# Optimization experiments

Hardware: AMD Instinct MI355X
Metric: run time of the kernel (lower is better)

## Reference

```python
import jax, jax.numpy as jnp
import numpy as np

N_KNOTS = 10
NEXPERTS = 1
NC = 8
STEP = 1.0 / (N_KNOTS - 1.0)
BN_EPS = 1e-5


def _spline_matrix(n, step):
    # natural cubic spline second-derivative solve matrix (precalc in torch code)
    mat = 4.0 * np.eye(n - 2)
    np.fill_diagonal(mat[1:, :-1], 1.0)
    np.fill_diagonal(mat[:-1, 1:], 1.0)
    A = 6.0 * np.linalg.inv(mat) / step ** 2
    z = np.zeros((1, n - 2))
    A = np.vstack([z, A, z])                      # [n, n-2]
    B = np.zeros((n - 2, n))
    np.fill_diagonal(B, 1.0)
    np.fill_diagonal(B[:, 1:], -2.0)
    np.fill_diagonal(B[:, 2:], 1.0)
    return jnp.asarray(A @ B, dtype=jnp.float32)  # [n, n]


def _conv(x, w, b, stride=2):
    y = jax.lax.conv_general_dilated(x, w, (stride, stride), 'VALID',
                                     dimension_numbers=('NCHW', 'OIHW', 'NCHW'))
    return y + b[None, :, None, None]


def _bn(x, g, be):
    # training-mode batchnorm (module default)
    m = x.mean(axis=(0, 2, 3), keepdims=True)
    v = x.var(axis=(0, 2, 3), keepdims=True)
    return g[None, :, None, None] * (x - m) * jax.lax.rsqrt(v + BN_EPS) + be[None, :, None, None]


def _interpolate(ys, mat):
    # ys: [..., n] -> cubic coeffs a,b,c,d each [..., n-1]
    h = STEP
    M = jnp.einsum('ij,...j->...i', mat, ys)
    a = (M[..., 1:] - M[..., :-1]) / (6.0 * h)
    b = M[..., :-1] / 2.0
    c = (ys[..., 1:] - ys[..., :-1]) / h - (M[..., 1:] + 2.0 * M[..., :-1]) * (h / 6.0)
    d = ys[..., :-1]
    return a, b, c, d


def _apply(coeffs, x):
    # coeffs: 4-tuple each [..., n-1]; x: [..., P] with matching leading dims
    a, b, c, d = coeffs
    xi = jnp.clip(jnp.floor(x / STEP), 0.0, N_KNOTS - 2.0)
    xf = x - xi * STEP
    idx = xi.astype(jnp.int32)
    ag = jnp.take_along_axis(a, idx, axis=-1)
    bg = jnp.take_along_axis(b, idx, axis=-1)
    cg = jnp.take_along_axis(c, idx, axis=-1)
    dg = jnp.take_along_axis(d, idx, axis=-1)
    return ((ag * xf + bg) * xf + cg) * xf + dg


def forward(x, w1, b1, w2, b2, g2, be2, w3, b3, g3, be3, w4, b4, g4, be4,
            w5, b5, g5, be5, fc1_w, fc1_b, fc2_w, fc2_b):
    B, C, H, W = x.shape
    small = x if (H, W) == (256, 256) else jax.image.resize(x, (B, C, 256, 256), 'bilinear')
    h = jax.nn.relu(_conv(small, w1, b1))
    h = _bn(jax.nn.relu(_conv(h, w2, b2)), g2, be2)
    h = _bn(jax.nn.relu(_conv(h, w3, b3)), g3, be3)
    h = _bn(jax.nn.relu(_conv(h, w4, b4)), g4, be4)
    h = _bn(jax.nn.relu(_conv(h, w5, b5)), g5, be5)   # [B, 16nc, 7, 7]
    h = h.mean(axis=(2, 3))                            # avgpool 7 -> [B, 16nc]
    h = jax.nn.relu(h @ fc1_w.T + fc1_b)
    ys = (h @ fc2_w.T + fc2_b).reshape(B, NEXPERTS, 3, N_KNOTS)
    identity = jnp.arange(N_KNOTS, dtype=jnp.float32) / (N_KNOTS - 1.0)
    ysn = ys + identity                                # residual spline
    mat = _spline_matrix(N_KNOTS, STEP)
    coeffs = _interpolate(ysn, mat)                    # each [B,E,3,n-1]
    # per-pixel spline eval at original resolution
    px = jnp.broadcast_to(x.reshape(B, 1, 3, H * W), (B, NEXPERTS, 3, H * W))
    out = _apply(coeffs, px).reshape(B, NEXPERTS, 3, H, W)
    out = jnp.transpose(out, (1, 0, 2, 3, 4))          # [E,B,3,H,W]
    # spline curves sampled at xs = arange(0,1,1/255) (255 points; detached in torch)
    xs = jnp.arange(0.0, 1.0, 1.0 / 255.0, dtype=jnp.float32)
    xs_b = jnp.broadcast_to(xs, (B, NEXPERTS, 3, xs.shape[0]))
    splines = jnp.transpose(_apply(coeffs, xs_b), (1, 0, 2, 3))  # [E,B,3,255]
    return out, splines


def setup_inputs() -> dict:
    key = jax.random.key(0)
    ks = jax.random.split(key, 16)
    n, nc, E = N_KNOTS, NC, NEXPERTS
    d = {}
    d['x'] = jax.random.uniform(ks[0], (8, 3, 1024, 1024), dtype=jnp.float32)
    d['w1'] = jax.random.normal(ks[1], (nc, 3, 3, 3), jnp.float32) * 0.1
    d['b1'] = jnp.zeros((nc,), jnp.float32)
    chans = [nc, 2 * nc, 4 * nc, 8 * nc, 16 * nc]
    for i, (ci, co) in enumerate(zip(chans[:-1], chans[1:]), start=2):
        d[f'w{i}'] = jax.random.normal(ks[i], (co, ci, 3, 3), jnp.float32) * 0.1
        d[f'b{i}'] = jnp.zeros((co,), jnp.float32)
        d[f'g{i}'] = jnp.ones((co,), jnp.float32)
        d[f'be{i}'] = jnp.zeros((co,), jnp.float32)
    d['fc1_w'] = jax.random.normal(ks[10], (16 * nc, 16 * nc), jnp.float32) * 0.05
    d['fc1_b'] = jnp.zeros((16 * nc,), jnp.float32)
    d['fc2_w'] = jax.random.normal(ks[11], (3 * n * E, 16 * nc), jnp.float32) * 0.05
    d['fc2_b'] = jnp.zeros((3 * n * E,), jnp.float32)
    return d


def reference(x, w1, b1, w2, b2, g2, be2, w3, b3, g3, be3, w4, b4, g4, be4,
              w5, b5, g5, be5, fc1_w, fc1_b, fc2_w, fc2_b):
    return forward(x, w1, b1, w2, b2, g2, be2, w3, b3, g3, be3, w4, b4, g4, be4,
                   w5, b5, g5, be5, fc1_w, fc1_b, fc2_w, fc2_b)
```

## Files before the change

### kernel.cpp

```cpp
#include <hip/hip_runtime.h>

#define SPLINE_OFF 25165824
#define STEP_F (1.0f/9.0f)

__global__ __launch_bounds__(256) void resize_k(const float* __restrict__ x,
                                                float* __restrict__ sm,
                                                float* __restrict__ wsz) {
    __shared__ float vsum[1024];
    const int blk = blockIdx.x;
    const int plane = blk >> 8;
    const int orow = blk & 255;
    const int t = threadIdx.x;
    if (blk == 0) {
        for (int i = t; i < 480; i += 256) wsz[i] = 0.f;
    }

    const float W[8] = {0.125f,0.375f,0.625f,0.875f,0.875f,0.625f,0.375f,0.125f};
    const float* p = x + (size_t)plane * 1048576 + t * 4;
    const int r0 = 4 * orow - 2;
    float ax = 0.f, ay = 0.f, az = 0.f, aw = 0.f;
    if (r0 >= 0 && r0 + 7 <= 1023) {
        #pragma unroll
        for (int k = 0; k < 8; k++) {
            const float4 v = *(const float4*)(p + (r0 + k) * 1024);
            const float w = W[k] * 0.25f;
            ax = fmaf(v.x, w, ax); ay = fmaf(v.y, w, ay);
            az = fmaf(v.z, w, az); aw = fmaf(v.w, w, aw);
        }
    } else {
        float wsum = 0.f;
        #pragma unroll
        for (int k = 0; k < 8; k++) {
            const int r = r0 + k;
            if (r >= 0 && r < 1024) {
                const float4 v = *(const float4*)(p + r * 1024);
                ax = fmaf(v.x, W[k], ax); ay = fmaf(v.y, W[k], ay);
                az = fmaf(v.z, W[k], az); aw = fmaf(v.w, W[k], aw);
                wsum += W[k];
            }
        }
        const float inv = 1.f / wsum;
        ax *= inv; ay *= inv; az *= inv; aw *= inv;
    }
    vsum[4 * t + 0] = ax; vsum[4 * t + 1] = ay;
    vsum[4 * t + 2] = az; vsum[4 * t + 3] = aw;
    __syncthreads();

    const int c0 = 4 * t - 2;
    float acc = 0.f;
    if (c0 >= 0 && c0 + 7 <= 1023) {
        #pragma unroll
        for (int k = 0; k < 8; k++)
            acc = fmaf(vsum[c0 + k], W[k] * 0.25f, acc);
    } else {
        float wsum = 0.f;
        #pragma unroll
        for (int k = 0; k < 8; k++) {
            const int c = c0 + k;
            if (c >= 0 && c < 1023 + 1) { if (c >= 0 && c < 1024) { acc = fmaf(vsum[c], W[k], acc); wsum += W[k]; } }
        }
        acc /= wsum;
    }
    sm[(size_t)blk * 256 + t] = acc;
}

template<int CIN, int COUT, int INW, int OUTW, int NCO, int CISPLIT, int PIX,
         bool INBN, bool STATS, bool SPATIAL, bool WRITE>
__global__ __launch_bounds__(PIX * CISPLIT) void conv_k(
    const float* __restrict__ in, const float* __restrict__ w,
    const float* __restrict__ bias,
    const float* __restrict__ g, const float* __restrict__ be,
    const float* __restrict__ inStats, float inInvN,
    float* __restrict__ out,
    float* __restrict__ gsum, float* __restrict__ gsumsq,
    float* __restrict__ spat)
{
    constexpr int BLOCK = PIX * CISPLIT;
    constexpr int CPS = CIN / CISPLIT;
    constexpr int COG = COUT / NCO;

    __shared__ float wsm[NCO][CIN * 9];
    __shared__ float scs[CIN], shs[CIN];
    __shared__ float wrow[NCO][CIN];
    __shared__ float cadd[NCO];
    __shared__ float part[CISPLIT][PIX][NCO];
    __shared__ float red[NCO][2][PIX / 64];

    const int tid = threadIdx.x;
    const int p   = tid & (PIX - 1);
    const int cs  = tid / PIX;
    const int bc  = blockIdx.y;
    const int b   = bc / COG;
    const int co0 = (bc % COG) * NCO;

    if constexpr (INBN) {
        for (int ci = tid; ci < CIN; ci += BLOCK) {
            float s  = inStats[ci];
            float sq = inStats[CIN + ci];
            float m  = s * inInvN;
            float v  = sq * inInvN - m * m;
            float sc = g[ci] * rsqrtf(v + 1e-5f);
            scs[ci] = sc;
            shs[ci] = be[ci] - m * sc;
        }
        __syncthreads();
    }

    for (int i = tid; i < NCO * CIN * 9; i += BLOCK) {
        int n = i / (CIN * 9), r = i - n * (CIN * 9), ci = r / 9;
        float wv = w[(co0 + n) * CIN * 9 + r];
        wsm[n][r] = INBN ? wv * scs[ci] : wv;
    }
    if constexpr (INBN) {
        for (int i = tid; i < NCO * CIN; i += BLOCK) {
            int n = i / CIN, ci = i - n * CIN;
            const float* wp = w + ((co0 + n) * CIN + ci) * 9;
            float s = 0.f;
            #pragma unroll
            for (int k = 0; k < 9; k++) s += wp[k];
            wrow[n][ci] = s;
        }
    }
    __syncthreads();
    if (tid < NCO) {
        float c = bias[co0 + tid];
        if constexpr (INBN) {
            for (int ci = 0; ci < CIN; ci++) c = fmaf(wrow[tid][ci], shs[ci], c);
        }
        cadd[tid] = c;
    }
    __syncthreads();

    const int npix = OUTW * OUTW;
    const int pg = blockIdx.x * PIX + p;
    float acc[NCO];
    #pragma unroll
    for (int n = 0; n < NCO; n++) acc[n] = 0.f;

    if (pg < npix) {
        const int oh = pg / OUTW, ow = pg - oh * OUTW;
        const float* ib = in + ((size_t)(b * CIN) + cs * CPS) * INW * INW
                             + (size_t)(2 * oh) * INW + 2 * ow;
        for (int ci = 0; ci < CPS; ci++) {
            const float* ip = ib + (size_t)ci * INW * INW;
            const int cw = (cs * CPS + ci) * 9;
            #pragma unroll
            for (int kh = 0; kh < 3; kh++) {
                const float* r = ip + kh * INW;
                #pragma unroll
                for (int kw = 0; kw < 3; kw++) {
                    const float xv = r[kw];
                    #pragma unroll
                    for (int n = 0; n < NCO; n++)
                        acc[n] = fmaf(xv, wsm[n][cw + kh * 3 + kw], acc[n]);
                }
            }
        }
    }

    float val[NCO];
    #pragma unroll
    for (int n = 0; n < NCO; n++) val[n] = 0.f;

    if constexpr (CISPLIT > 1) {
        #pragma unroll
        for (int n = 0; n < NCO; n++) part[cs][p][n] = acc[n];
        __syncthreads();
    }

    if (cs == 0) {
        #pragma unroll
        for (int n = 0; n < NCO; n++) {
            float s = acc[n];
            if constexpr (CISPLIT > 1) {
                #pragma unroll
                for (int q = 1; q < CISPLIT; q++) s += part[q][p][n];
            }
            if (pg < npix) {
                val[n] = fmaxf(s + cadd[n], 0.f);
                if constexpr (WRITE)
                    out[(size_t)(b * COUT + co0 + n) * npix + pg] = val[n];
            }
        }
    }

    if constexpr (STATS) {
        if (cs == 0) {
            #pragma unroll
            for (int n = 0; n < NCO; n++) {
                float s = val[n], sq = val[n] * val[n];
                #pragma unroll
                for (int off = 32; off > 0; off >>= 1) {
                    s  += __shfl_down(s, off);
                    sq += __shfl_down(sq, off);
                }
                if ((tid & 63) == 0) { red[n][0][tid >> 6] = s; red[n][1][tid >> 6] = sq; }
            }
        }
        __syncthreads();
        if (tid == 0) {
            #pragma unroll
            for (int n = 0; n < NCO; n++) {
                float ts = 0.f, tq = 0.f;
                #pragma unroll
                for (int i = 0; i < PIX / 64; i++) { ts += red[n][0][i]; tq += red[n][1][i]; }
                atomicAdd(&gsum[co0 + n], ts);
                atomicAdd(&gsumsq[co0 + n], tq);
                if constexpr (SPATIAL) spat[b * COUT + co0 + n] = ts;
            }
        }
    }
}

__global__ __launch_bounds__(256) void fc_spline_k(
    const float* __restrict__ spat5, const float* __restrict__ stats5,
    const float* __restrict__ g5, const float* __restrict__ be5,
    const float* __restrict__ fc1w, const float* __restrict__ fc1b,
    const float* __restrict__ fc2w, const float* __restrict__ fc2b,
    float* __restrict__ coeff_out, float* __restrict__ splines_out)
{
    __shared__ float sc5[128], sh5[128];
    __shared__ float h[1024];
    __shared__ float h1v[1024];
    __shared__ float ysn[240];
    __shared__ float coef[24][36];

    const int t = threadIdx.x;

    if (t < 128) {
        float m = stats5[t] * (1.f / 392.f);
        float v = stats5[128 + t] * (1.f / 392.f) - m * m;
        float sc = g5[t] * rsqrtf(v + 1e-5f);
        sc5[t] = sc;
        sh5[t] = be5[t] - m * sc;
    }
    __syncthreads();

    for (int i = t; i < 1024; i += 256) {
        int c = i & 127;
        h[i] = fmaf(sc5[c], spat5[i] * (1.f / 49.f), sh5[c]);
    }
    __syncthreads();

    for (int i = t; i < 1024; i += 256) {
        int b = i >> 7, j = i & 127;
        float acc = fc1b[j];
        for (int c = 0; c < 128; c++)
            acc = fmaf(h[(b << 7) + c], fc1w[(j << 7) + c], acc);
        h1v[i] = fmaxf(acc, 0.f);
    }
    __syncthreads();

    if (t < 240) {
        int b = t / 30, k = t % 30;
        float acc = fc2b[k];
        for (int j = 0; j < 128; j++)
            acc = fmaf(h1v[(b << 7) + j], fc2w[(k << 7) + j], acc);
        ysn[t] = acc + (float)(k % 10) * STEP_F;
    }
    __syncthreads();

    if (t < 24) {
        float y[10];
        #pragma unroll
        for (int i = 0; i < 10; i++) y[i] = ysn[t * 10 + i];
        float rhs[9], cp[9], dp[9];
        #pragma unroll
        for (int i = 1; i <= 8; i++)
            rhs[i] = 486.f * (y[i - 1] - 2.f * y[i] + y[i + 1]);
        cp[1] = 0.25f; dp[1] = rhs[1] * 0.25f;
        #pragma unroll
        for (int i = 2; i <= 8; i++) {
            float m = 1.f / (4.f - cp[i - 1]);
            cp[i] = m;
            dp[i] = (rhs[i] - dp[i - 1]) * m;
        }
        float M[10];
        M[0] = 0.f; M[9] = 0.f;
        M[8] = dp[8];
        #pragma unroll
        for (int i = 7; i >= 1; i--) M[i] = dp[i] - cp[i] * M[i + 1];
        #pragma unroll
        for (int i = 0; i < 9; i++) {
            float a = (M[i + 1] - M[i]) * 1.5f;
            float bb = M[i] * 0.5f;
            float cc = (y[i + 1] - y[i]) * 9.f - (M[i + 1] + 2.f * M[i]) * (STEP_F / 6.f);
            float dd = y[i];
            coef[t][i] = a; coef[t][9 + i] = bb; coef[t][18 + i] = cc; coef[t][27 + i] = dd;
            coeff_out[t * 36 + i] = a;
            coeff_out[t * 36 + 9 + i] = bb;
            coeff_out[t * 36 + 18 + i] = cc;
            coeff_out[t * 36 + 27 + i] = dd;
        }
    }
    __syncthreads();

    for (int i = t; i < 24 * 255; i += 256) {
        int bc = i / 255, k = i - bc * 255;
        float xv = (float)k * (1.0f / 255.0f);
        float xi = floorf(xv * 9.0f);
        xi = fminf(fmaxf(xi, 0.f), 8.f);
        int ix = (int)xi;
        float xf = xv - xi * STEP_F;
        const float* cf = coef[bc];
        splines_out[i] = fmaf(fmaf(fmaf(cf[ix], xf, cf[9 + ix]), xf, cf[18 + ix]), xf, cf[27 + ix]);
    }
}

__global__ __launch_bounds__(256) void apply_k(const float* __restrict__ x,
                                               const float* __restrict__ coeff,
                                               float* __restrict__ out)
{
    __shared__ float cf[36];
    const int blk = blockIdx.x;
    const int plane = blk >> 10;
    const int t = threadIdx.x;
    if (t < 36) cf[t] = coeff[plane * 36 + t];
    __syncthreads();

    size_t base = (size_t)blk * 1024 + (size_t)t * 4;
    float4 v = *(const float4*)(x + base);
    float4 o;
    #pragma unroll
    for (int k = 0; k < 4; k++) {
        float xv = (k == 0) ? v.x : (k == 1) ? v.y : (k == 2) ? v.z : v.w;
        float xi = floorf(xv * 9.0f);
        xi = fminf(fmaxf(xi, 0.f), 8.f);
        int ix = (int)xi;
        float xf = xv - xi * STEP_F;
        float r = fmaf(fmaf(fmaf(cf[ix], xf, cf[9 + ix]), xf, cf[18 + ix]), xf, cf[27 + ix]);
        if (k == 0) o.x = r; else if (k == 1) o.y = r; else if (k == 2) o.z = r; else o.w = r;
    }
    *(float4*)(out + base) = o;
}

extern "C" void kernel_launch(void* const* d_in, const int* in_sizes, int n_in,
                              void* d_out, int out_size, void* d_ws, size_t ws_size,
                              hipStream_t stream) {
    (void)in_sizes; (void)n_in; (void)out_size; (void)ws_size;

    const float* x    = (const float*)d_in[0];
    const float* w1   = (const float*)d_in[1];
    const float* b1   = (const float*)d_in[2];
    const float* w2   = (const float*)d_in[3];
    const float* b2   = (const float*)d_in[4];
    const float* g2   = (const float*)d_in[5];
    const float* be2  = (const float*)d_in[6];
    const float* w3   = (const float*)d_in[7];
    const float* b3   = (const float*)d_in[8];
    const float* g3   = (const float*)d_in[9];
    const float* be3  = (const float*)d_in[10];
    const float* w4   = (const float*)d_in[11];
    const float* b4   = (const float*)d_in[12];
    const float* g4   = (const float*)d_in[13];
    const float* be4  = (const float*)d_in[14];
    const float* w5   = (const float*)d_in[15];
    const float* b5   = (const float*)d_in[16];
    const float* g5   = (const float*)d_in[17];
    const float* be5  = (const float*)d_in[18];
    const float* fc1w = (const float*)d_in[19];
    const float* fc1b = (const float*)d_in[20];
    const float* fc2w = (const float*)d_in[21];
    const float* fc2b = (const float*)d_in[22];

    float* out = (float*)d_out;
    float* wsf = (float*)d_ws;

    float* stats2 = wsf + 0;
    float* stats3 = wsf + 32;
    float* stats4 = wsf + 96;
    float* stats5 = wsf + 224;
    float* spat5  = wsf + 480;
    float* coeff  = wsf + 1504;

    float* sm  = out;
    float* h1  = out + 1572864;
    float* h2  = out + 2605120;
    float* h3  = out + 3113152;
    float* h4  = out + 3359168;

    resize_k<<<6144, 256, 0, stream>>>(x, sm, wsf);

    conv_k<3, 8, 256, 127, 2, 1, 256, false, false, false, true>
        <<<dim3(64, 32), 256, 0, stream>>>(sm, w1, b1, nullptr, nullptr, nullptr, 0.f,
                                           h1, nullptr, nullptr, nullptr);
    conv_k<8, 16, 127, 63, 2, 1, 256, false, true, false, true>
        <<<dim3(16, 64), 256, 0, stream>>>(h1, w2, b2, nullptr, nullptr, nullptr, 0.f,
                                           h2, stats2, stats2 + 16, nullptr);
    conv_k<16, 32, 63, 31, 2, 1, 256, true, true, false, true>
        <<<dim3(4, 128), 256, 0, stream>>>(h2, w3, b3, g2, be2, stats2, 1.0f / 31752.0f,
                                           h3, stats3, stats3 + 32, nullptr);
    conv_k<32, 64, 31, 15, 2, 2, 256, true, true, false, true>
        <<<dim3(1, 256), 512, 0, stream>>>(h3, w4, b4, g3, be3, stats3, 1.0f / 7688.0f,
                                           h4, stats4, stats4 + 64, nullptr);
    conv_k<64, 128, 15, 7, 2, 4, 64, true, true, true, false>
        <<<dim3(1, 512), 256, 0, stream>>>(h4, w5, b5, g4, be4, stats4, 1.0f / 1800.0f,
                                           nullptr, stats5, stats5 + 128, spat5);

    fc_spline_k<<<1, 256, 0, stream>>>(spat5, stats5, g5, be5,
                                       fc1w, fc1b, fc2w, fc2b,
                                       coeff, out + SPLINE_OFF);

    apply_k<<<24576, 256, 0, stream>>>(x, coeff, out);
}
```

Before: 157.4 us.

## Replace atomic BN stats with per-block partial sums reduced by consumers

```diff
diff --git a/kernel.cpp b/kernel.cpp
--- a/kernel.cpp
+++ b/kernel.cpp
@@ -3,17 +3,15 @@
 #define SPLINE_OFF 25165824
 #define STEP_F (1.0f/9.0f)
 
+typedef float f32x4 __attribute__((ext_vector_type(4)));
+
 __global__ __launch_bounds__(256) void resize_k(const float* __restrict__ x,
-                                                float* __restrict__ sm,
-                                                float* __restrict__ wsz) {
+                                                float* __restrict__ sm) {
     __shared__ float vsum[1024];
     const int blk = blockIdx.x;
     const int plane = blk >> 8;
     const int orow = blk & 255;
     const int t = threadIdx.x;
-    if (blk == 0) {
-        for (int i = t; i < 480; i += 256) wsz[i] = 0.f;
-    }
 
     const float W[8] = {0.125f,0.375f,0.625f,0.875f,0.875f,0.625f,0.375f,0.125f};
     const float* p = x + (size_t)plane * 1048576 + t * 4;
@@ -57,7 +55,7 @@
         #pragma unroll
         for (int k = 0; k < 8; k++) {
             const int c = c0 + k;
-            if (c >= 0 && c < 1023 + 1) { if (c >= 0 && c < 1024) { acc = fmaf(vsum[c], W[k], acc); wsum += W[k]; } }
+            if (c >= 0 && c < 1024) { acc = fmaf(vsum[c], W[k], acc); wsum += W[k]; }
         }
         acc /= wsum;
     }
@@ -65,15 +63,14 @@
 }
 
 template<int CIN, int COUT, int INW, int OUTW, int NCO, int CISPLIT, int PIX,
-         bool INBN, bool STATS, bool SPATIAL, bool WRITE>
+         int NTPREV, int NTOUT, bool INBN, bool STATS, bool WRITE>
 __global__ __launch_bounds__(PIX * CISPLIT) void conv_k(
     const float* __restrict__ in, const float* __restrict__ w,
     const float* __restrict__ bias,
-    const float* __restrict__ g, const float* __restrict__ be,
-    const float* __restrict__ inStats, float inInvN,
+    const float* __restrict__ gam, const float* __restrict__ be,
+    const float* __restrict__ pS, const float* __restrict__ pQ, float invN,
     float* __restrict__ out,
-    float* __restrict__ gsum, float* __restrict__ gsumsq,
-    float* __restrict__ spat)
+    float* __restrict__ pSo, float* __restrict__ pQo)
 {
     constexpr int BLOCK = PIX * CISPLIT;
     constexpr int CPS = CIN / CISPLIT;
@@ -85,6 +82,7 @@
     __shared__ float cadd[NCO];
     __shared__ float part[CISPLIT][PIX][NCO];
     __shared__ float red[NCO][2][PIX / 64];
+    __shared__ float sredS[BLOCK], sredQ[BLOCK];
 
     const int tid = threadIdx.x;
     const int p   = tid & (PIX - 1);
@@ -94,14 +92,31 @@
     const int co0 = (bc % COG) * NCO;
 
     if constexpr (INBN) {
-        for (int ci = tid; ci < CIN; ci += BLOCK) {
-            float s  = inStats[ci];
-            float sq = inStats[CIN + ci];
-            float m  = s * inInvN;
-            float v  = sq * inInvN - m * m;
-            float sc = g[ci] * rsqrtf(v + 1e-5f);
-            scs[ci] = sc;
-            shs[ci] = be[ci] - m * sc;
+        constexpr int GRP = BLOCK / CIN;
+        constexpr int TERMS = 8 * NTPREV;
+        const int ci = tid % CIN;
+        const int gi = tid / CIN;
+        float s = 0.f, q = 0.f;
+        for (int j = gi; j < TERMS; j += GRP) {
+            const int bb = j / NTPREV, tl = j - bb * NTPREV;
+            const int a = (bb * CIN + ci) * NTPREV + tl;
+            s += pS[a]; q += pQ[a];
+        }
+        sredS[gi * CIN + ci] = s;
+        sredQ[gi * CIN + ci] = q;
+        __syncthreads();
+        if (tid < CIN) {
+            float ts = 0.f, tq = 0.f;
+            #pragma unroll
+            for (int g2 = 0; g2 < GRP; g2++) {
+                ts += sredS[g2 * CIN + tid];
+                tq += sredQ[g2 * CIN + tid];
+            }
+            const float m = ts * invN;
+            const float v = tq * invN - m * m;
+            const float sc = gam[tid] * rsqrtf(v + 1e-5f);
+            scs[tid] = sc;
+            shs[tid] = be[tid] - m * sc;
         }
         __syncthreads();
     }
@@ -141,6 +156,7 @@
         const int oh = pg / OUTW, ow = pg - oh * OUTW;
         const float* ib = in + ((size_t)(b * CIN) + cs * CPS) * INW * INW
                              + (size_t)(2 * oh) * INW + 2 * ow;
+        #pragma unroll 4
         for (int ci = 0; ci < CPS; ci++) {
             const float* ip = ib + (size_t)ci * INW * INW;
             const int cw = (cs * CPS + ci) * 9;
@@ -204,16 +220,16 @@
                 float ts = 0.f, tq = 0.f;
                 #pragma unroll
                 for (int i = 0; i < PIX / 64; i++) { ts += red[n][0][i]; tq += red[n][1][i]; }
-                atomicAdd(&gsum[co0 + n], ts);
-                atomicAdd(&gsumsq[co0 + n], tq);
-                if constexpr (SPATIAL) spat[b * COUT + co0 + n] = ts;
+                const int idx = (b * COUT + co0 + n) * NTOUT + blockIdx.x;
+                pSo[idx] = ts;
+                pQo[idx] = tq;
             }
         }
     }
 }
 
 __global__ __launch_bounds__(256) void fc_spline_k(
-    const float* __restrict__ spat5, const float* __restrict__ stats5,
+    const float* __restrict__ pS5, const float* __restrict__ pQ5,
     const float* __restrict__ g5, const float* __restrict__ be5,
     const float* __restrict__ fc1w, const float* __restrict__ fc1b,
     const float* __restrict__ fc2w, const float* __restrict__ fc2b,
@@ -228,8 +244,11 @@
     const int t = threadIdx.x;
 
     if (t < 128) {
-        float m = stats5[t] * (1.f / 392.f);
-        float v = stats5[128 + t] * (1.f / 392.f) - m * m;
+        float s = 0.f, q = 0.f;
+        #pragma unroll
+        for (int b = 0; b < 8; b++) { s += pS5[b * 128 + t]; q += pQ5[b * 128 + t]; }
+        float m = s * (1.f / 392.f);
+        float v = q * (1.f / 392.f) - m * m;
         float sc = g5[t] * rsqrtf(v + 1e-5f);
         sc5[t] = sc;
         sh5[t] = be5[t] - m * sc;
@@ -238,7 +257,7 @@
 
     for (int i = t; i < 1024; i += 256) {
         int c = i & 127;
-        h[i] = fmaf(sc5[c], spat5[i] * (1.f / 49.f), sh5[c]);
+        h[i] = fmaf(sc5[c], pS5[i] * (1.f / 49.f), sh5[c]);
     }
     __syncthreads();
 
@@ -320,7 +339,7 @@
 
     size_t base = (size_t)blk * 1024 + (size_t)t * 4;
     float4 v = *(const float4*)(x + base);
-    float4 o;
+    f32x4 o;
     #pragma unroll
     for (int k = 0; k < 4; k++) {
         float xv = (k == 0) ? v.x : (k == 1) ? v.y : (k == 2) ? v.z : v.w;
@@ -328,10 +347,9 @@
         xi = fminf(fmaxf(xi, 0.f), 8.f);
         int ix = (int)xi;
         float xf = xv - xi * STEP_F;
-        float r = fmaf(fmaf(fmaf(cf[ix], xf, cf[9 + ix]), xf, cf[18 + ix]), xf, cf[27 + ix]);
-        if (k == 0) o.x = r; else if (k == 1) o.y = r; else if (k == 2) o.z = r; else o.w = r;
-    }
-    *(float4*)(out + base) = o;
+        o[k] = fmaf(fmaf(fmaf(cf[ix], xf, cf[9 + ix]), xf, cf[18 + ix]), xf, cf[27 + ix]);
+    }
+    __builtin_nontemporal_store(o, (f32x4*)(out + base));
 }
 
 extern "C" void kernel_launch(void* const* d_in, const int* in_sizes, int n_in,
@@ -366,12 +384,15 @@
     float* out = (float*)d_out;
     float* wsf = (float*)d_ws;
 
-    float* stats2 = wsf + 0;
-    float* stats3 = wsf + 32;
-    float* stats4 = wsf + 96;
-    float* stats5 = wsf + 224;
-    float* spat5  = wsf + 480;
-    float* coeff  = wsf + 1504;
+    float* pS2 = wsf + 0;
+    float* pQ2 = wsf + 2048;
+    float* pS3 = wsf + 4096;
+    float* pQ3 = wsf + 5120;
+    float* pS4 = wsf + 6144;
+    float* pQ4 = wsf + 6656;
+    float* pS5 = wsf + 7168;
+    float* pQ5 = wsf + 8192;
+    float* coeff = wsf + 9216;
 
     float* sm  = out;
     float* h1  = out + 1572864;
@@ -379,25 +400,30 @@
     float* h3  = out + 3113152;
     float* h4  = out + 3359168;
 
-    resize_k<<<6144, 256, 0, stream>>>(x, sm, wsf);
-
-    conv_k<3, 8, 256, 127, 2, 1, 256, false, false, false, true>
-        <<<dim3(64, 32), 256, 0, stream>>>(sm, w1, b1, nullptr, nullptr, nullptr, 0.f,
-                                           h1, nullptr, nullptr, nullptr);
-    conv_k<8, 16, 127, 63, 2, 1, 256, false, true, false, true>
-        <<<dim3(16, 64), 256, 0, stream>>>(h1, w2, b2, nullptr, nullptr, nullptr, 0.f,
-                                           h2, stats2, stats2 + 16, nullptr);
-    conv_k<16, 32, 63, 31, 2, 1, 256, true, true, false, true>
-        <<<dim3(4, 128), 256, 0, stream>>>(h2, w3, b3, g2, be2, stats2, 1.0f / 31752.0f,
-                                           h3, stats3, stats3 + 32, nullptr);
-    conv_k<32, 64, 31, 15, 2, 2, 256, true, true, false, true>
-        <<<dim3(1, 256), 512, 0, stream>>>(h3, w4, b4, g3, be3, stats3, 1.0f / 7688.0f,
-                                           h4, stats4, stats4 + 64, nullptr);
-    conv_k<64, 128, 15, 7, 2, 4, 64, true, true, true, false>
-        <<<dim3(1, 512), 256, 0, stream>>>(h4, w5, b5, g4, be4, stats4, 1.0f / 1800.0f,
-                                           nullptr, stats5, stats5 + 128, spat5);
-
-    fc_spline_k<<<1, 256, 0, stream>>>(spat5, stats5, g5, be5,
+    resize_k<<<6144, 256, 0, stream>>>(x, sm);
+
+    conv_k<3, 8, 256, 127, 2, 1, 256, 1, 1, false, false, true>
+        <<<dim3(64, 32), 256, 0, stream>>>(sm, w1, b1, nullptr, nullptr,
+                                           nullptr, nullptr, 0.f,
+                                           h1, nullptr, nullptr);
+    conv_k<8, 16, 127, 63, 2, 1, 256, 1, 16, false, true, true>
+        <<<dim3(16, 64), 256, 0, stream>>>(h1, w2, b2, nullptr, nullptr,
+                                           nullptr, nullptr, 0.f,
+                                           h2, pS2, pQ2);
+    conv_k<16, 32, 63, 31, 2, 1, 256, 16, 4, true, true, true>
+        <<<dim3(4, 128), 256, 0, stream>>>(h2, w3, b3, g2, be2,
+                                           pS2, pQ2, 1.0f / 31752.0f,
+                                           h3, pS3, pQ3);
+    conv_k<32, 64, 31, 15, 2, 2, 256, 4, 1, true, true, true>
+        <<<dim3(1, 256), 512, 0, stream>>>(h3, w4, b4, g3, be3,
+                                           pS3, pQ3, 1.0f / 7688.0f,
+                                           h4, pS4, pQ4);
+    conv_k<64, 128, 15, 7, 2, 4, 64, 1, 1, true, true, false>
+        <<<dim3(1, 512), 256, 0, stream>>>(h4, w5, b5, g4, be4,
+                                           pS4, pQ4, 1.0f / 1800.0f,
+                                           nullptr, pS5, pQ5);
+
+    fc_spline_k<<<1, 256, 0, stream>>>(pS5, pQ5, g5, be5,
                                        fc1w, fc1b, fc2w, fc2b,
                                        coeff, out + SPLINE_OFF);
 
```

Result: faster. 132.1 us (-16.1%).
